# Kernel tuning notes

Measured on AMD Instinct MI355X. Metric: run time of the kernel, lower is better.

Reference implementation:

```python
import jax, jax.numpy as jnp
import numpy as np

B, L, D = 8, 2048, 256
D_MODEL = 1024
NUM_SIGNALS = 16
MAX_POSITIONS = 4096
ROLE_OUTPUT = 2  # role id used for the CLS token


def setup_inputs() -> dict:
    key = jax.random.key(0)
    ks = jax.random.split(key, 12)
    emb = jax.random.normal(ks[0], (B, L, D), dtype=jnp.float32)
    pos = jax.random.randint(ks[1], (B, L), 1, MAX_POSITIONS + 1)          # pos >= 1 for real tokens
    sid = jax.random.randint(ks[2], (B, L), 0, NUM_SIGNALS)
    role = jax.random.randint(ks[3], (B, L), 0, 3)
    padding_mask = jax.random.uniform(ks[4], (B, L)) < 0.75                # True = real token
    # learned parameters
    proj_W = jax.random.normal(ks[5], (NUM_SIGNALS, D_MODEL, D), dtype=jnp.float32) * (1.0 / np.sqrt(D))
    proj_b = jax.random.normal(ks[6], (NUM_SIGNALS, D_MODEL), dtype=jnp.float32) * 0.01
    cls_content = jax.random.normal(ks[7], (D_MODEL,), dtype=jnp.float32)
    pos_embed = jax.random.normal(ks[8], (MAX_POSITIONS + 1, D_MODEL), dtype=jnp.float32)
    id_embed = jax.random.normal(ks[9], (NUM_SIGNALS + 1, D_MODEL), dtype=jnp.float32)
    role_embed = jax.random.normal(ks[10], (3, D_MODEL), dtype=jnp.float32)
    return dict(emb=emb, pos=pos, sid=sid, role=role, padding_mask=padding_mask,
                proj_W=proj_W, proj_b=proj_b, cls_content=cls_content,
                pos_embed=pos_embed, id_embed=id_embed, role_embed=role_embed)


def reference(emb, pos, sid, role, padding_mask,
              proj_W, proj_b, cls_content, pos_embed, id_embed, role_embed):
    Bv, Lv, _ = emb.shape
    S, d_model, _ = proj_W.shape
    cls_id = S

    # Grouped per-signal projection: one GEMM per signal id, select per token.
    tokens = jnp.zeros((Bv, Lv, d_model), dtype=emb.dtype)
    for s in range(S):
        proj_s = jnp.einsum('bld,ed->ble', emb, proj_W[s]) + proj_b[s]   # (B, L, d_model)
        keep = ((sid == s) & padding_mask)[..., None]
        tokens = jnp.where(keep, proj_s, tokens)

    # Prepend CLS
    cls = jnp.broadcast_to(cls_content[None, None, :], (Bv, 1, d_model))
    tokens = jnp.concatenate([cls, tokens], axis=1)                       # (B, L+1, d_model)

    pos_full = jnp.concatenate([jnp.zeros((Bv, 1), dtype=pos.dtype), pos], axis=1)
    sid_full = jnp.concatenate([jnp.full((Bv, 1), cls_id, dtype=sid.dtype), sid], axis=1)
    role_full = jnp.concatenate([jnp.full((Bv, 1), ROLE_OUTPUT, dtype=role.dtype), role], axis=1)

    tokens = tokens + pos_embed[pos_full] + id_embed[sid_full] + role_embed[role_full]

    attn_keep = jnp.concatenate([jnp.ones((Bv, 1), dtype=bool), padding_mask], axis=1)
    return tokens, attn_keep
```

## Files before the change

kernel.cpp:

```cpp
#include <hip/hip_runtime.h>
#include <hip/hip_bf16.h>
#include <stdint.h>

#define B_ 8
#define L_ 2048
#define NTOK 16384
#define DK 256
#define DM 1024
#define NS 16
#define LOUT 2049
#define TOK_OUT (B_*LOUT*DM)
#define ATTN_OUT (B_*LOUT)

typedef unsigned short u16;
typedef unsigned int u32;
typedef __bf16 bf16x8 __attribute__((ext_vector_type(8)));
typedef float f32x4 __attribute__((ext_vector_type(4)));

__device__ inline u32 packbf2(float lo, float hi) {
    u32 a, b;
    __builtin_memcpy(&a, &lo, 4);
    __builtin_memcpy(&b, &hi, 4);
    a = (a + 0x8000u) >> 16;
    b = (b + 0x8000u) & 0xFFFF0000u;
    return a | b;
}

#define WS_CNT 0
#define WS_CUR 16
#define WS_PERM 64
#define WS_MASK (64 + NTOK)

__global__ __launch_bounds__(256) void p1_kernel(const unsigned char* __restrict__ mb,
                                                 const int* __restrict__ sid,
                                                 int* __restrict__ wsi) {
    __shared__ int f_c1ge2, f_ge2, f_odd;
    __shared__ int lcnt[NS];
    int tid = threadIdx.x;
    if (tid == 0) { f_c1ge2 = 0; f_ge2 = 0; f_odd = 0; }
    if (tid < NS) lcnt[tid] = 0;
    __syncthreads();

    int c1ge2 = 0, ge2 = 0, oddnz = 0;
    const u32* mw = (const u32*)mb;
    #pragma unroll
    for (int i = 0; i < 16; i++) {
        u32 x = mw[tid * 16 + i];
        u32 b0 = x & 0xFF, b1 = (x >> 8) & 0xFF, b2 = (x >> 16) & 0xFF, b3 = x >> 24;
        if (b1 >= 2) c1ge2 = 1;
        if (b0 >= 2 || b1 >= 2 || b2 >= 2 || b3 >= 2) ge2 = 1;
        if ((b1 | b3) != 0) oddnz = 1;
    }
    if (c1ge2) atomicOr(&f_c1ge2, 1);
    if (ge2) atomicOr(&f_ge2, 1);
    if (oddnz) atomicOr(&f_odd, 1);
    __syncthreads();

    int width;
    if (f_c1ge2) width = 2;
    else if (f_ge2) width = 4;
    else if (f_odd) width = 1;
    else width = 4;

    int t = blockIdx.x * 256 + tid;
    int m;
    if (width == 1) m = (mb[t] != 0);
    else if (width == 2) m = (((const u16*)mb)[t] != 0);
    else m = (((const u32*)mb)[t] != 0);

    wsi[WS_MASK + t] = m;
    if (m) atomicAdd(&lcnt[sid[t]], 1);
    __syncthreads();
    if (tid < NS) atomicAdd(&wsi[WS_CNT + tid], lcnt[tid]);
}

__global__ __launch_bounds__(256) void p3_kernel(const int* __restrict__ sid,
                                                 int* __restrict__ wsi) {
    __shared__ int gcnt[NS], lcnt[NS], base[NS];
    int tid = threadIdx.x;
    if (tid < NS) { gcnt[tid] = wsi[WS_CNT + tid]; lcnt[tid] = 0; }
    __syncthreads();
    int t = blockIdx.x * 256 + tid;
    int m = wsi[WS_MASK + t];
    int s = sid[t];
    int r = 0;
    if (m) r = atomicAdd(&lcnt[s], 1);
    __syncthreads();
    if (tid < NS) {
        int off = 0;
        for (int i = 0; i < tid; i++) off += gcnt[i];
        base[tid] = off + atomicAdd(&wsi[WS_CUR + tid], lcnt[tid]);
    }
    __syncthreads();
    if (m) wsi[WS_PERM + base[s] + r] = t;
}

#define SP 136

__global__ __launch_bounds__(256) void gemm_kernel(
    const float* __restrict__ emb, const int* __restrict__ pos,
    const int* __restrict__ role,
    const float* __restrict__ W, const float* __restrict__ bias,
    const float* __restrict__ pos_emb, const float* __restrict__ id_emb,
    const float* __restrict__ role_emb,
    const int* __restrict__ wsi, float* __restrict__ out) {
    __shared__ u16 As[64 * SP];
    __shared__ u16 Bs[64 * SP];
    __shared__ int toks[64];
    int tid = threadIdx.x;

    int cnts[NS];
    #pragma unroll
    for (int i = 0; i < NS; i++) cnts[i] = wsi[WS_CNT + i];
    int ry = (int)blockIdx.y;
    int s = -1, tokOff = 0, lrt = 0;
    #pragma unroll
    for (int i = 0; i < NS; i++) {
        int rt = (cnts[i] + 63) >> 6;
        if (s < 0) {
            if (ry < rt) { s = i; lrt = ry; }
            else { ry -= rt; tokOff += cnts[i]; }
        }
    }
    if (s < 0) return;
    int idx0 = tokOff + lrt * 64;
    int v = cnts[s] - lrt * 64;
    if (v > 64) v = 64;

    if (tid < 64) toks[tid] = (tid < v) ? wsi[WS_PERM + idx0 + tid] : -1;
    __syncthreads();

    int lane = tid & 63;
    int w = tid >> 6;
    int mcol = lane & 15;
    int quad = lane >> 4;
    int n0 = (int)blockIdx.x * 64;

    f32x4 acc[4];
    #pragma unroll
    for (int j = 0; j < 4; j++) acc[j] = (f32x4){0.f, 0.f, 0.f, 0.f};

    const float* Wbase = W + (size_t)s * DM * DK + (size_t)n0 * DK;

    for (int kc = 0; kc < 2; ++kc) {
        #pragma unroll
        for (int i = 0; i < 8; i++) {
            int q = tid + 256 * i;
            int row = q >> 5, seg = q & 31;
            int t = toks[row];
            float4 a = make_float4(0.f, 0.f, 0.f, 0.f);
            if (t >= 0) a = *(const float4*)(emb + (size_t)t * DK + kc * 128 + seg * 4);
            uint2 ap;
            ap.x = packbf2(a.x, a.y);
            ap.y = packbf2(a.z, a.w);
            *(uint2*)(As + row * SP + seg * 4) = ap;
        }
        #pragma unroll
        for (int i = 0; i < 8; i++) {
            int q = tid + 256 * i;
            int row = q >> 5, seg = q & 31;
            float4 b = *(const float4*)(Wbase + (size_t)row * DK + kc * 128 + seg * 4);
            uint2 bp;
            bp.x = packbf2(b.x, b.y);
            bp.y = packbf2(b.z, b.w);
            *(uint2*)(Bs + row * SP + seg * 4) = bp;
        }
        __syncthreads();
        #pragma unroll
        for (int ks = 0; ks < 4; ++ks) {
            int kk = ks * 32 + quad * 8;
            bf16x8 af = *(const bf16x8*)(As + (16 * w + mcol) * SP + kk);
            #pragma unroll
            for (int j = 0; j < 4; j++) {
                bf16x8 bfr = *(const bf16x8*)(Bs + (16 * j + mcol) * SP + kk);
                acc[j] = __builtin_amdgcn_mfma_f32_16x16x32_bf16(af, bfr, acc[j], 0, 0, 0);
            }
        }
        __syncthreads();
    }

    #pragma unroll
    for (int r = 0; r < 4; r++) {
        int mrow = 16 * w + quad * 4 + r;
        if (mrow >= v) continue;
        int t = toks[mrow];
        int p = pos[t];
        int ro = role[t];
        int b = t >> 11, l = t & 2047;
        size_t orow = (size_t)(b * LOUT + l + 1) * DM;
        #pragma unroll
        for (int j = 0; j < 4; j++) {
            int col = n0 + 16 * j + mcol;
            float val = acc[j][r]
                + bias[s * DM + col]
                + pos_emb[(size_t)p * DM + col]
                + id_emb[s * DM + col]
                + role_emb[ro * DM + col];
            out[orow + col] = val;
        }
    }
}

__global__ __launch_bounds__(256) void ew_kernel(
    const int* __restrict__ pos, const int* __restrict__ sid,
    const int* __restrict__ role,
    const float* __restrict__ cls, const float* __restrict__ pos_emb,
    const float* __restrict__ id_emb, const float* __restrict__ role_emb,
    const int* __restrict__ wsi, float* __restrict__ out) {
    int bi = blockIdx.x;
    int tid = threadIdx.x;
    if (bi < NTOK) {
        int t = bi;
        if (wsi[WS_MASK + t]) return;
        int p = pos[t], sd = sid[t], ro = role[t];
        int b = t >> 11, l = t & 2047;
        size_t orow = (size_t)(b * LOUT + l + 1) * DM;
        int c = tid * 4;
        float4 a = *(const float4*)(pos_emb + (size_t)p * DM + c);
        float4 d = *(const float4*)(id_emb + (size_t)sd * DM + c);
        float4 e = *(const float4*)(role_emb + (size_t)ro * DM + c);
        float4 o;
        o.x = a.x + d.x + e.x;
        o.y = a.y + d.y + e.y;
        o.z = a.z + d.z + e.z;
        o.w = a.w + d.w + e.w;
        *(float4*)(out + orow + c) = o;
    } else if (bi < NTOK + B_) {
        int b = bi - NTOK;
        size_t orow = (size_t)(b * LOUT) * DM;
        int c = tid * 4;
        float4 cc = *(const float4*)(cls + c);
        float4 a = *(const float4*)(pos_emb + c);
        float4 d = *(const float4*)(id_emb + NS * DM + c);
        float4 e = *(const float4*)(role_emb + 2 * DM + c);
        float4 o;
        o.x = cc.x + a.x + d.x + e.x;
        o.y = cc.y + a.y + d.y + e.y;
        o.z = cc.z + a.z + d.z + e.z;
        o.w = cc.w + a.w + d.w + e.w;
        *(float4*)(out + orow + c) = o;
    } else {
        int i = (bi - NTOK - B_) * 256 + tid;
        if (i < ATTN_OUT) {
            int b = i / LOUT;
            int j = i - b * LOUT;
            float val = (j == 0) ? 1.0f : (float)wsi[WS_MASK + b * L_ + j - 1];
            out[TOK_OUT + i] = val;
        }
    }
}

extern "C" void kernel_launch(void* const* d_in, const int* in_sizes, int n_in,
                              void* d_out, int out_size, void* d_ws, size_t ws_size,
                              hipStream_t stream) {
    const float* emb = (const float*)d_in[0];
    const int* pos = (const int*)d_in[1];
    const int* sid = (const int*)d_in[2];
    const int* role = (const int*)d_in[3];
    const unsigned char* mask = (const unsigned char*)d_in[4];
    const float* W = (const float*)d_in[5];
    const float* bias = (const float*)d_in[6];
    const float* cls = (const float*)d_in[7];
    const float* pos_emb = (const float*)d_in[8];
    const float* id_emb = (const float*)d_in[9];
    const float* role_emb = (const float*)d_in[10];
    float* out = (float*)d_out;
    int* wsi = (int*)d_ws;

    hipMemsetAsync(wsi, 0, 32 * sizeof(int), stream);
    hipLaunchKernelGGL(p1_kernel, dim3(64), dim3(256), 0, stream, mask, sid, wsi);
    hipLaunchKernelGGL(p3_kernel, dim3(64), dim3(256), 0, stream, sid, wsi);
    hipLaunchKernelGGL(gemm_kernel, dim3(16, 272), dim3(256), 0, stream,
                       emb, pos, role, W, bias, pos_emb, id_emb, role_emb, wsi, out);
    hipLaunchKernelGGL(ew_kernel, dim3(NTOK + B_ + 65), dim3(256), 0, stream,
                       pos, sid, role, cls, pos_emb, id_emb, role_emb, wsi, out);
}
```

Baseline: 180.9 us.

## Pre-convert gathered A and W to bf16 in workspace and use 128x128 MFMA GEMM

Adds a prep kernel that gathers the tokens of each signal into padded contiguous bf16 rows and converts the weights to bf16 in the workspace. A new 128x128-tile GEMM then loads these tiles with global_load_lds direct-to-LDS copies into an XOR-swizzled layout and runs bf16 MFMA. The goal is to drop the per-tile fp32 conversion and gather work inside the GEMM and to increase data reuse. The cost is an extra pass over emb and W plus a workspace-size requirement. The old kernel is kept as a fallback when the workspace is too small.

```diff
diff --git a/kernel.cpp b/kernel.cpp
--- a/kernel.cpp
+++ b/kernel.cpp
@@ -26,10 +26,20 @@
     return a | b;
 }
 
+__device__ inline void gll16(const void* g, void* l) {
+    __builtin_amdgcn_global_load_lds(
+        (const __attribute__((address_space(1))) unsigned int*)g,
+        (__attribute__((address_space(3))) unsigned int*)l, 16, 0, 0);
+}
+
 #define WS_CNT 0
 #define WS_CUR 16
 #define WS_PERM 64
 #define WS_MASK (64 + NTOK)
+#define A_OFF 262144ULL
+#define APAD_ROWS 18432
+#define W_OFF (A_OFF + (unsigned long long)APAD_ROWS * 512ULL)
+#define WS_NEED (W_OFF + 16384ULL * 512ULL)
 
 __global__ __launch_bounds__(256) void p1_kernel(const unsigned char* __restrict__ mb,
                                                  const int* __restrict__ sid,
@@ -95,9 +105,173 @@
     if (m) wsi[WS_PERM + base[s] + r] = t;
 }
 
+__global__ __launch_bounds__(256) void prep_kernel(const float* __restrict__ emb,
+                                                   const float* __restrict__ W,
+                                                   int* __restrict__ wsi,
+                                                   unsigned char* __restrict__ wsb) {
+    int bid = blockIdx.x;
+    int tid = threadIdx.x;
+    int lane = tid & 63;
+    int wv = tid >> 6;
+    if (bid < 4608) {
+        int cnts[NS], segoff[NS], pbase[NS];
+        int accp = 0, accu = 0;
+        #pragma unroll
+        for (int i = 0; i < NS; i++) {
+            cnts[i] = wsi[WS_CNT + i];
+            segoff[i] = accp; pbase[i] = accu;
+            accp += ((cnts[i] + 127) >> 7) << 7;
+            accu += cnts[i];
+        }
+        int r = bid * 4 + wv;
+        if (r >= accp) return;
+        int s = 0;
+        #pragma unroll
+        for (int i = 1; i < NS; i++) if (r >= segoff[i]) s = i;
+        int local = r - segoff[s];
+        u16* Ab = (u16*)(wsb + A_OFF);
+        uint2 o;
+        if (local < cnts[s]) {
+            int t = wsi[WS_PERM + pbase[s] + local];
+            float4 a = *(const float4*)(emb + (size_t)t * DK + lane * 4);
+            o.x = packbf2(a.x, a.y);
+            o.y = packbf2(a.z, a.w);
+        } else {
+            o.x = 0; o.y = 0;
+        }
+        *(uint2*)(Ab + (size_t)r * DK + lane * 4) = o;
+    } else {
+        int r = (bid - 4608) * 4 + wv;
+        u16* Wb = (u16*)(wsb + W_OFF);
+        float4 a = *(const float4*)(W + (size_t)r * DK + lane * 4);
+        uint2 o;
+        o.x = packbf2(a.x, a.y);
+        o.y = packbf2(a.z, a.w);
+        *(uint2*)(Wb + (size_t)r * DK + lane * 4) = o;
+    }
+}
+
+__global__ __launch_bounds__(256) void gemm_big(
+    const int* __restrict__ pos, const int* __restrict__ role,
+    const float* __restrict__ bias,
+    const float* __restrict__ pos_emb, const float* __restrict__ id_emb,
+    const float* __restrict__ role_emb,
+    const int* __restrict__ wsi, const unsigned char* __restrict__ wsb,
+    float* __restrict__ out) {
+    __shared__ u16 As[128 * 64];
+    __shared__ u16 Bs[128 * 64];
+    __shared__ int toks[128];
+    int tid = threadIdx.x;
+    int lane = tid & 63;
+    int wv = tid >> 6;
+
+    int cnts[NS];
+    #pragma unroll
+    for (int i = 0; i < NS; i++) cnts[i] = wsi[WS_CNT + i];
+    int ry = (int)blockIdx.y;
+    int s = -1, lrt = 0, seg0 = 0, pb = 0;
+    {
+        int accp = 0, accu = 0;
+        #pragma unroll
+        for (int i = 0; i < NS; i++) {
+            int rt = (cnts[i] + 127) >> 7;
+            if (s < 0) {
+                if (ry < rt) { s = i; lrt = ry; seg0 = accp; pb = accu; }
+                else ry -= rt;
+            }
+            accp += rt << 7;
+            accu += cnts[i];
+        }
+    }
+    if (s < 0) return;
+    int rowsValid = cnts[s] - lrt * 128;
+    if (rowsValid > 128) rowsValid = 128;
+
+    if (tid < 128) toks[tid] = (tid < rowsValid) ? wsi[WS_PERM + pb + lrt * 128 + tid] : -1;
+
+    int n0 = (int)blockIdx.x * 128;
+    const u16* Ab = (const u16*)(wsb + A_OFF) + (size_t)(seg0 + lrt * 128) * DK;
+    const u16* Bb = (const u16*)(wsb + W_OFF) + (size_t)(s * DM + n0) * DK;
+
+    int srow = lane >> 3;
+    int sseg = (lane & 7) ^ srow;
+
+    f32x4 acc[4][4];
+    #pragma unroll
+    for (int im = 0; im < 4; im++)
+        #pragma unroll
+        for (int jn = 0; jn < 4; jn++) acc[im][jn] = (f32x4){0.f, 0.f, 0.f, 0.f};
+
+    int wm = wv >> 1, wn = wv & 1;
+    int mcol = lane & 15;
+    int quad = lane >> 4;
+
+    for (int kc = 0; kc < 4; ++kc) {
+        #pragma unroll
+        for (int i = 0; i < 4; i++) {
+            int row = wv * 32 + i * 8;
+            gll16(Ab + (size_t)(row + srow) * DK + kc * 64 + sseg * 8,
+                  As + row * 64);
+            gll16(Bb + (size_t)(row + srow) * DK + kc * 64 + sseg * 8,
+                  Bs + row * 64);
+        }
+        __syncthreads();
+        #pragma unroll
+        for (int ks = 0; ks < 2; ++ks) {
+            bf16x8 af[4], bf[4];
+            #pragma unroll
+            for (int im = 0; im < 4; im++) {
+                int row = wm * 64 + im * 16 + mcol;
+                int sg = (ks * 4 + quad) ^ (row & 7);
+                af[im] = *(const bf16x8*)(As + row * 64 + sg * 8);
+            }
+            #pragma unroll
+            for (int jn = 0; jn < 4; jn++) {
+                int row = wn * 64 + jn * 16 + mcol;
+                int sg = (ks * 4 + quad) ^ (row & 7);
+                bf[jn] = *(const bf16x8*)(Bs + row * 64 + sg * 8);
+            }
+            #pragma unroll
+            for (int im = 0; im < 4; im++)
+                #pragma unroll
+                for (int jn = 0; jn < 4; jn++)
+                    acc[im][jn] = __builtin_amdgcn_mfma_f32_16x16x32_bf16(
+                        af[im], bf[jn], acc[im][jn], 0, 0, 0);
+        }
+        __syncthreads();
+    }
+
+    float bc[4];
+    #pragma unroll
+    for (int jn = 0; jn < 4; jn++) {
+        int col = n0 + wn * 64 + jn * 16 + mcol;
+        bc[jn] = bias[s * DM + col] + id_emb[s * DM + col];
+    }
+    #pragma unroll
+    for (int im = 0; im < 4; im++) {
+        #pragma unroll
+        for (int r = 0; r < 4; r++) {
+            int rowT = wm * 64 + im * 16 + quad * 4 + r;
+            if (rowT >= rowsValid) continue;
+            int t = toks[rowT];
+            int p = pos[t];
+            int ro = role[t];
+            int b = t >> 11, l = t & 2047;
+            size_t orow = (size_t)(b * LOUT + l + 1) * DM;
+            #pragma unroll
+            for (int jn = 0; jn < 4; jn++) {
+                int col = n0 + wn * 64 + jn * 16 + mcol;
+                float val = acc[im][jn][r] + bc[jn]
+                    + pos_emb[(size_t)p * DM + col]
+                    + role_emb[ro * DM + col];
+                out[orow + col] = val;
+            }
+        }
+    }
+}
+
 #define SP 136
-
-__global__ __launch_bounds__(256) void gemm_kernel(
+__global__ __launch_bounds__(256) void gemm_small(
     const float* __restrict__ emb, const int* __restrict__ pos,
     const int* __restrict__ role,
     const float* __restrict__ W, const float* __restrict__ bias,
@@ -266,12 +440,20 @@
     const float* role_emb = (const float*)d_in[10];
     float* out = (float*)d_out;
     int* wsi = (int*)d_ws;
+    unsigned char* wsb = (unsigned char*)d_ws;
 
     hipMemsetAsync(wsi, 0, 32 * sizeof(int), stream);
     hipLaunchKernelGGL(p1_kernel, dim3(64), dim3(256), 0, stream, mask, sid, wsi);
     hipLaunchKernelGGL(p3_kernel, dim3(64), dim3(256), 0, stream, sid, wsi);
-    hipLaunchKernelGGL(gemm_kernel, dim3(16, 272), dim3(256), 0, stream,
-                       emb, pos, role, W, bias, pos_emb, id_emb, role_emb, wsi, out);
+    if (ws_size >= WS_NEED) {
+        hipLaunchKernelGGL(prep_kernel, dim3(4608 + 4096), dim3(256), 0, stream,
+                           emb, W, wsi, wsb);
+        hipLaunchKernelGGL(gemm_big, dim3(8, 144), dim3(256), 0, stream,
+                           pos, role, bias, pos_emb, id_emb, role_emb, wsi, wsb, out);
+    } else {
+        hipLaunchKernelGGL(gemm_small, dim3(16, 272), dim3(256), 0, stream,
+                           emb, pos, role, W, bias, pos_emb, id_emb, role_emb, wsi, out);
+    }
     hipLaunchKernelGGL(ew_kernel, dim3(NTOK + B_ + 65), dim3(256), 0, stream,
                        pos, sid, role, cls, pos_emb, id_emb, role_emb, wsi, out);
 }
```

Measured after the change: 171.8 us. -5.0%, faster.
